# Kernel tuning notes

Measured on AMD Instinct MI355X. Metric: run time of the kernel, lower is better.

The kernel has to match this reference:

```python
import jax, jax.numpy as jnp
import numpy as np

EPS = 1e-5
NUM_GROUPS = 32

def _nin(x, w, b):
    # 1x1 conv: x (B,C,H,W), w (K,C), b (K,)
    return jnp.einsum('bchw,kc->bkhw', x, w) + b[None, :, None, None]

def _group_norm(x, gamma, beta, num_groups=NUM_GROUPS, eps=EPS):
    B, C, H, W = x.shape
    xg = x.reshape(B, num_groups, C // num_groups, H, W)
    mean = xg.mean(axis=(2, 3, 4), keepdims=True)
    var = xg.var(axis=(2, 3, 4), keepdims=True)
    xg = (xg - mean) * jax.lax.rsqrt(var + eps)
    x = xg.reshape(B, C, H, W)
    return x * gamma[None, :, None, None] + beta[None, :, None, None]

def setup_inputs() -> dict:
    key = jax.random.key(0)
    ks = jax.random.split(key, 10)
    B, C, H, W = 8, 512, 64, 64
    att = 512
    s = 0.02
    return {
        'x': jax.random.normal(ks[0], (B, C, H, W), dtype=jnp.float32),
        'gn_weight': jnp.ones((C,), jnp.float32),
        'gn_bias': jnp.zeros((C,), jnp.float32),
        'q_w': jax.random.normal(ks[1], (att, C), jnp.float32) * s,
        'q_b': jnp.zeros((att,), jnp.float32),
        'k_w': jax.random.normal(ks[2], (att, C), jnp.float32) * s,
        'k_b': jnp.zeros((att,), jnp.float32),
        'v_w': jax.random.normal(ks[3], (att, C), jnp.float32) * s,
        'v_b': jnp.zeros((att,), jnp.float32),
        'proj_w': jax.random.normal(ks[4], (C, att), jnp.float32) * s,
        'proj_b': jnp.zeros((C,), jnp.float32),
    }

def reference(x, gn_weight, gn_bias, q_w, q_b, k_w, k_b, v_w, v_b, proj_w, proj_b):
    B, C, H, W = x.shape
    h = _group_norm(x, gn_weight, gn_bias)
    q = _nin(h, q_w, q_b)  # (B, D, H, W)
    k = _nin(h, k_w, k_b)
    v = _nin(h, v_w, v_b)
    N = H * W
    qf = q.reshape(B, -1, N)
    kf = k.reshape(B, -1, N)
    vf = v.reshape(B, -1, N)
    scale = C ** (-0.5)  # note: scaled by input channel C, per source
    w = jnp.einsum('bdn,bdm->bnm', qf, kf) * scale  # (B, N, N)
    w = jax.nn.softmax(w, axis=-1)
    hf = jnp.einsum('bnm,bdm->bdn', w, vf)
    h = hf.reshape(B, -1, H, W)
    h = _nin(h, proj_w, proj_b)
    return x + h
```

## Files before the change

kernel.cpp:

```cpp
#include <hip/hip_runtime.h>
#include <hip/hip_bf16.h>
#include <cstdint>
#include <cstddef>

typedef __bf16 bf16_t;
typedef __bf16 bf16x8 __attribute__((ext_vector_type(8)));
typedef __bf16 bf16x4 __attribute__((ext_vector_type(4)));
typedef float f32x4 __attribute__((ext_vector_type(4)));

__device__ __forceinline__ void async16(const void* g, void* l) {
  __builtin_amdgcn_global_load_lds(
      (const __attribute__((address_space(1))) void*)g,
      (__attribute__((address_space(3))) void*)l,
      16, 0, 0);
}

__global__ __launch_bounds__(256) void f2b4(const float* __restrict__ w0,
                                            const float* __restrict__ w1,
                                            const float* __restrict__ w2,
                                            const float* __restrict__ w3,
                                            bf16_t* __restrict__ o0,
                                            bf16_t* __restrict__ o1,
                                            bf16_t* __restrict__ o2,
                                            bf16_t* __restrict__ o3) {
  const float* in = (blockIdx.y == 0) ? w0 : (blockIdx.y == 1) ? w1
                   : (blockIdx.y == 2) ? w2 : w3;
  bf16_t* out = (blockIdx.y == 0) ? o0 : (blockIdx.y == 1) ? o1
               : (blockIdx.y == 2) ? o2 : o3;
  const int i = blockIdx.x * 256 + threadIdx.x;
  float4 v = ((const float4*)in)[i];
  bf16x4 o = { (__bf16)v.x, (__bf16)v.y, (__bf16)v.z, (__bf16)v.w };
  ((bf16x4*)out)[i] = o;
}

__global__ __launch_bounds__(256) void groupnorm_t(const float* __restrict__ x,
                                                   const float* __restrict__ gamma,
                                                   const float* __restrict__ beta,
                                                   bf16_t* __restrict__ ht) {
  const int g = blockIdx.x;
  const int b = blockIdx.y;
  const int t = threadIdx.x;
  const float* xg = x + ((size_t)(b * 512 + g * 16)) * 4096;
  const float4* x4 = (const float4*)xg;

  float s = 0.f, ss = 0.f;
  #pragma unroll 8
  for (int i = t; i < 16384; i += 256) {
    float4 v = x4[i];
    s  += (v.x + v.y) + (v.z + v.w);
    ss += (v.x * v.x + v.y * v.y) + (v.z * v.z + v.w * v.w);
  }
  #pragma unroll
  for (int o = 32; o; o >>= 1) { s += __shfl_xor(s, o); ss += __shfl_xor(ss, o); }
  __shared__ float rs[4], rss[4];
  if ((t & 63) == 0) { rs[t >> 6] = s; rss[t >> 6] = ss; }
  __syncthreads();
  const float S  = (rs[0] + rs[1]) + (rs[2] + rs[3]);
  const float SS = (rss[0] + rss[1]) + (rss[2] + rss[3]);
  const float inv_n = 1.0f / 65536.0f;
  const float mean = S * inv_n;
  const float var  = SS * inv_n - mean * mean;
  const float rstd = rsqrtf(var + 1e-5f);

  float ga[16], be[16];
  #pragma unroll
  for (int cc = 0; cc < 16; cc++) {
    const float gm = gamma[g * 16 + cc] * rstd;
    ga[cc] = gm;
    be[cc] = beta[g * 16 + cc] - mean * gm;
  }

  bf16_t* hg = ht + (size_t)b * 4096 * 512 + g * 16;
  for (int n = t; n < 4096; n += 256) {
    bf16_t o[16];
    #pragma unroll
    for (int cc = 0; cc < 16; cc++)
      o[cc] = (bf16_t)(xg[(size_t)cc * 4096 + n] * ga[cc] + be[cc]);
    bf16x8* dst = (bf16x8*)(hg + (size_t)n * 512);
    dst[0] = *(bf16x8*)&o[0];
    dst[1] = *(bf16x8*)&o[8];
  }
}

template <int OUTF32, int BIAS_MODE, int RESID, int SWAP>
__global__ __launch_bounds__(256)
void gemm_bt(const bf16_t* __restrict__ A, const bf16_t* __restrict__ B,
             void* __restrict__ Cv, const float* __restrict__ bias,
             const float* __restrict__ resid,
             int TM, int TN, int Z, int K, float scale,
             long sA, long sB, long sC, long sR) {
  __shared__ alignas(16) bf16_t lA[4096];
  __shared__ alignas(16) bf16_t lB[4096];

  const int lid = blockIdx.x;
  const int xcd = lid & 7;
  const int j   = lid >> 3;
  const int sd  = SWAP ? TN : TM;
  const int I   = SWAP ? TM : TN;
  const int spx = (sd * Z) >> 3;
  const int strip = xcd * spx + j / I;
  const int inner = j % I;
  const int z    = strip / sd;
  const int sidx = strip % sd;
  const int bm = (SWAP ? inner : sidx) * 128;
  const int bn = (SWAP ? sidx : inner) * 128;
  const int N = TN * 128;

  const int t = threadIdx.x;
  const int lane = t & 63;
  const int w = t >> 6;
  const int wm = (w >> 1) * 64;
  const int wn = (w & 1) * 64;
  const bf16_t* Ab = A + (size_t)z * (size_t)sA;
  const bf16_t* Bb = B + (size_t)z * (size_t)sB;

  const int lrow = lane >> 2;
  const int lcol = (lane & 3) * 8;
  const int quad = lane >> 4;
  const int l15 = lane & 15;

  const bf16_t* gA0 = Ab + (size_t)(bm + w * 16 + lrow) * K + lcol;
  const bf16_t* gA1 = Ab + (size_t)(bm + (w + 4) * 16 + lrow) * K + lcol;
  const bf16_t* gB0 = Bb + (size_t)(bn + w * 16 + lrow) * K + lcol;
  const bf16_t* gB1 = Bb + (size_t)(bn + (w + 4) * 16 + lrow) * K + lcol;
  bf16_t* lA0 = &lA[w * 512];
  bf16_t* lA1 = &lA[(w + 4) * 512];
  bf16_t* lB0 = &lB[w * 512];
  bf16_t* lB1 = &lB[(w + 4) * 512];

  f32x4 acc[4][4] = {};

  for (int k0 = 0; k0 < K; k0 += 32) {
    __syncthreads();
    async16(gA0 + k0, lA0);
    async16(gA1 + k0, lA1);
    async16(gB0 + k0, lB0);
    async16(gB1 + k0, lB1);
    __syncthreads();

    bf16x8 af[4], bfr[4];
    #pragma unroll
    for (int i = 0; i < 4; i++) {
      af[i]  = *(const bf16x8*)&lA[(wm + i * 16 + l15) * 32 + quad * 8];
      bfr[i] = *(const bf16x8*)&lB[(wn + i * 16 + l15) * 32 + quad * 8];
    }
    #pragma unroll
    for (int i = 0; i < 4; i++)
      #pragma unroll
      for (int jj = 0; jj < 4; jj++)
        acc[i][jj] = __builtin_amdgcn_mfma_f32_16x16x32_bf16(af[i], bfr[jj],
                                                             acc[i][jj], 0, 0, 0);
  }

  float* Cf = (float*)Cv + (size_t)z * (size_t)sC;
  bf16_t* Cb = (bf16_t*)Cv + (size_t)z * (size_t)sC;
  const float* Rb = RESID ? (resid + (size_t)z * (size_t)sR) : nullptr;

  #pragma unroll
  for (int i = 0; i < 4; i++) {
    const int row0 = bm + wm + i * 16 + quad * 4;
    #pragma unroll
    for (int jj = 0; jj < 4; jj++) {
      const int col = bn + wn + jj * 16 + l15;
      #pragma unroll
      for (int r = 0; r < 4; r++) {
        float v = acc[i][jj][r] * scale;
        const int row = row0 + r;
        if (BIAS_MODE == 1) v += bias[row];
        else if (BIAS_MODE == 2) v += bias[col];
        const size_t idx = (size_t)row * N + col;
        if (RESID) v += Rb[idx];
        if (OUTF32) Cf[idx] = v;
        else Cb[idx] = (bf16_t)v;
      }
    }
  }
}

__global__ __launch_bounds__(512, 2)
void flash_attn(const bf16_t* __restrict__ Qm, const bf16_t* __restrict__ Km,
                const bf16_t* __restrict__ Vm, bf16_t* __restrict__ Om,
                float scale) {
  __shared__ alignas(16) bf16_t lT[2][4][128][32];
  __shared__ alignas(16) bf16_t lS[8][16][144];
  __shared__ float lL[8][16];

  const int bid = blockIdx.x;
  const int z = bid & 7;
  const int qb = bid >> 3;
  const int m0 = qb * 128;

  const int t = threadIdx.x;
  const int lane = t & 63;
  const int w = t >> 6;
  const int quad = lane >> 4;
  const int l15 = lane & 15;
  const int srow = lane >> 2;
  const int scol = (lane & 3) * 8;
  const int g2 = w & 6;
  const int dh = w & 1;

  const size_t sND = 4096ull * 512;
  const bf16_t* q = Qm + z * sND;
  const bf16_t* k = Km + z * sND;
  const bf16_t* v = Vm + z * sND;

  const bf16_t* kStage = k + (size_t)(w * 16 + srow) * 512 + scol;
  const bf16_t* vStage = v + (size_t)(w * 16 + srow) * 4096 + scol;

  bf16x8 qf[16];
  {
    const bf16_t* qrow = q + (size_t)(m0 + w * 16 + l15) * 512 + quad * 8;
    #pragma unroll
    for (int kk = 0; kk < 16; kk++)
      qf[kk] = *(const bf16x8*)(qrow + kk * 32);
  }

  f32x4 o_acc[32] = {};
  float l_run[4] = {0.f, 0.f, 0.f, 0.f};
  f32x4 s_acc[8];

  auto stageA = [&](int BUF, int kcc, int kd2) __attribute__((always_inline)) {
    #pragma unroll
    for (int c = 0; c < 4; c++)
      async16(kStage + (size_t)kcc * 512 + kd2 * 128 + c * 32,
              &lT[BUF][c][w * 16][0]);
  };
  auto stageC = [&](int BUF, int kcc, int db) __attribute__((always_inline)) {
    #pragma unroll
    for (int c = 0; c < 4; c++)
      async16(vStage + (size_t)db * 128 * 4096 + kcc + c * 32,
              &lT[BUF][c][w * 16][0]);
  };
  auto computeA = [&](int BUF, int kd2) __attribute__((always_inline)) {
    #pragma unroll
    for (int p = 0; p < 4; p++)
      #pragma unroll
      for (int n = 0; n < 8; n++) {
        bf16x8 kf = *(const bf16x8*)&lT[BUF][p][n * 16 + l15][quad * 8];
        s_acc[n] = __builtin_amdgcn_mfma_f32_16x16x32_bf16(
            qf[kd2 * 4 + p], kf, s_acc[n], 0, 0, 0);
      }
  };
  auto computeC = [&](int BUF, int db) __attribute__((always_inline)) {
    #pragma unroll
    for (int p = 0; p < 4; p++) {
      bf16x8 af0 = *(const bf16x8*)&lS[g2][l15][p * 32 + quad * 8];
      bf16x8 af1 = *(const bf16x8*)&lS[g2 + 1][l15][p * 32 + quad * 8];
      #pragma unroll
      for (int nd = 0; nd < 4; nd++) {
        bf16x8 vf = *(const bf16x8*)&lT[BUF][p][dh * 64 + nd * 16 + l15][quad * 8];
        o_acc[db * 8 + nd] = __builtin_amdgcn_mfma_f32_16x16x32_bf16(
            af0, vf, o_acc[db * 8 + nd], 0, 0, 0);
        o_acc[db * 8 + 4 + nd] = __builtin_amdgcn_mfma_f32_16x16x32_bf16(
            af1, vf, o_acc[db * 8 + 4 + nd], 0, 0, 0);
      }
    }
  };
  auto phaseB = [&]() __attribute__((always_inline)) {
    float lsum[4] = {0.f, 0.f, 0.f, 0.f};
    #pragma unroll
    for (int n = 0; n < 8; n++)
      #pragma unroll
      for (int r = 0; r < 4; r++) {
        float e = __expf(s_acc[n][r] * scale);
        lsum[r] += e;
        lS[w][quad * 4 + r][n * 16 + l15] = (bf16_t)e;
      }
    #pragma unroll
    for (int r = 0; r < 4; r++) {
      float s = lsum[r];
      s += __shfl_xor(s, 1); s += __shfl_xor(s, 2);
      s += __shfl_xor(s, 4); s += __shfl_xor(s, 8);
      l_run[r] += s;
    }
  };

  stageA(0, 0, 0);
  __syncthreads();

  for (int kc = 0; kc < 4096; kc += 128) {
    #pragma unroll
    for (int n = 0; n < 8; n++) s_acc[n] = (f32x4){0.f, 0.f, 0.f, 0.f};

    stageA(1, kc, 1);  computeA(0, 0);            __syncthreads();
    stageA(0, kc, 2);  computeA(1, 1);            __syncthreads();
    stageA(1, kc, 3);  computeA(0, 2);            __syncthreads();
    stageC(0, kc, 0);  computeA(1, 3);  phaseB(); __syncthreads();
    stageC(1, kc, 1);  computeC(0, 0);            __syncthreads();
    stageC(0, kc, 2);  computeC(1, 1);            __syncthreads();
    stageC(1, kc, 3);  computeC(0, 2);            __syncthreads();
    if (kc + 128 < 4096) stageA(0, kc + 128, 0);
    computeC(1, 3);                               __syncthreads();
  }

  if (l15 == 0) {
    #pragma unroll
    for (int r = 0; r < 4; r++) lL[w][quad * 4 + r] = l_run[r];
  }
  __syncthreads();
  float rl[2][4];
  #pragma unroll
  for (int s = 0; s < 2; s++)
    #pragma unroll
    for (int r = 0; r < 4; r++) rl[s][r] = 1.0f / lL[g2 + s][quad * 4 + r];

  bf16_t* o = Om + z * sND;
  #pragma unroll
  for (int db = 0; db < 4; db++)
    #pragma unroll
    for (int s = 0; s < 2; s++)
      #pragma unroll
      for (int nd = 0; nd < 4; nd++)
        #pragma unroll
        for (int r = 0; r < 4; r++) {
          const int row = m0 + (g2 + s) * 16 + quad * 4 + r;
          const int col = db * 128 + dh * 64 + nd * 16 + l15;
          o[(size_t)row * 512 + col] =
              (bf16_t)(o_acc[db * 8 + s * 4 + nd][r] * rl[s][r]);
        }
}

extern "C" void kernel_launch(void* const* d_in, const int* in_sizes, int n_in,
                              void* d_out, int out_size, void* d_ws, size_t ws_size,
                              hipStream_t stream) {
  const float* x   = (const float*)d_in[0];
  const float* gnw = (const float*)d_in[1];
  const float* gnb = (const float*)d_in[2];
  const float* qw  = (const float*)d_in[3];
  const float* qb  = (const float*)d_in[4];
  const float* kw  = (const float*)d_in[5];
  const float* kb  = (const float*)d_in[6];
  const float* vw  = (const float*)d_in[7];
  const float* vb  = (const float*)d_in[8];
  const float* pw  = (const float*)d_in[9];
  const float* pb  = (const float*)d_in[10];
  float* out = (float*)d_out;

  char* ws = (char*)d_ws;
  size_t off = 0;
  auto alloc = [&](size_t bytes) -> void* {
    void* p = ws + off;
    off += (bytes + 255) & ~(size_t)255;
    return p;
  };

  const long sND = 4096L * 512;

  bf16_t* wqb = (bf16_t*)alloc(512ull * 512 * 2);
  bf16_t* wkb = (bf16_t*)alloc(512ull * 512 * 2);
  bf16_t* wvb = (bf16_t*)alloc(512ull * 512 * 2);
  bf16_t* wpb = (bf16_t*)alloc(512ull * 512 * 2);
  bf16_t* ht  = (bf16_t*)alloc(8ull * 4096 * 512 * 2);
  bf16_t* qbf = (bf16_t*)alloc(8ull * 4096 * 512 * 2);
  bf16_t* kbf = (bf16_t*)alloc(8ull * 4096 * 512 * 2);
  bf16_t* vbf = (bf16_t*)alloc(8ull * 4096 * 512 * 2);
  bf16_t* hfb = ht;

  f2b4<<<dim3(256, 4), 256, 0, stream>>>(qw, kw, vw, pw, wqb, wkb, wvb, wpb);
  groupnorm_t<<<dim3(32, 8), 256, 0, stream>>>(x, gnw, gnb, ht);

  gemm_bt<0, 2, 0, 0><<<1024, 256, 0, stream>>>(
      ht, wqb, qbf, qb, nullptr, 32, 4, 8, 512, 1.0f, sND, 0, sND, 0);
  gemm_bt<0, 2, 0, 0><<<1024, 256, 0, stream>>>(
      ht, wkb, kbf, kb, nullptr, 32, 4, 8, 512, 1.0f, sND, 0, sND, 0);
  gemm_bt<0, 1, 0, 1><<<1024, 256, 0, stream>>>(
      wvb, ht, vbf, vb, nullptr, 4, 32, 8, 512, 1.0f, 0, sND, sND, 0);

  const float scale = 0.044194173824159216f;
  flash_attn<<<256, 512, 0, stream>>>(qbf, kbf, vbf, hfb, scale);

  gemm_bt<1, 1, 1, 1><<<1024, 256, 0, stream>>>(
      wpb, hfb, out, pb, x, 4, 32, 8, 512, 1.0f, 0, sND, 512L * 4096, 512L * 4096);
}
```

Baseline: 661.4 us.

## Split attention keys across two wave groups with smaller query tiles

The flash attention kernel now processes 64 query rows per block instead of 128 and splits each 128-key chunk between two groups of four waves, each holding its own half of the key/value tiles. Partial output accumulators and row sums are combined through shared memory at the end, and the grid doubles to 512 blocks. The score scratch is XOR-swizzled to avoid LDS bank conflicts. The intent is more blocks for better CU occupancy and load balance, at the cost of a shared-memory reduction epilogue, extra barriers, and Q being re-read by twice as many blocks.

After: 756.2 us. 1.14x slower.

```diff
diff --git a/kernel.cpp b/kernel.cpp
--- a/kernel.cpp
+++ b/kernel.cpp
@@ -181,20 +181,22 @@
 void flash_attn(const bf16_t* __restrict__ Qm, const bf16_t* __restrict__ Km,
                 const bf16_t* __restrict__ Vm, bf16_t* __restrict__ Om,
                 float scale) {
-  __shared__ alignas(16) bf16_t lT[2][4][128][32];
-  __shared__ alignas(16) bf16_t lS[8][16][144];
-  __shared__ float lL[8][16];
+  __shared__ alignas(16) bf16_t lT[2][2][8192];
+  __shared__ alignas(16) bf16_t lS[8][16][64];
 
   const int bid = blockIdx.x;
   const int z = bid & 7;
   const int qb = bid >> 3;
-  const int m0 = qb * 128;
+  const int m0 = qb * 64;
 
   const int t = threadIdx.x;
   const int lane = t & 63;
   const int w = t >> 6;
+  const int ws = w & 3;
+  const int kh = w >> 2;
   const int quad = lane >> 4;
   const int l15 = lane & 15;
+  const int l7 = l15 & 7;
   const int srow = lane >> 2;
   const int scol = (lane & 3) * 8;
   const int g2 = w & 6;
@@ -205,12 +207,12 @@
   const bf16_t* k = Km + z * sND;
   const bf16_t* v = Vm + z * sND;
 
-  const bf16_t* kStage = k + (size_t)(w * 16 + srow) * 512 + scol;
-  const bf16_t* vStage = v + (size_t)(w * 16 + srow) * 4096 + scol;
+  const bf16_t* kStage = k + (size_t)(ws * 16 + srow) * 512 + scol;
+  const bf16_t* vStage = v + (size_t)(ws * 32 + srow) * 4096 + scol;
 
   bf16x8 qf[16];
   {
-    const bf16_t* qrow = q + (size_t)(m0 + w * 16 + l15) * 512 + quad * 8;
+    const bf16_t* qrow = q + (size_t)(m0 + ws * 16 + l15) * 512 + quad * 8;
     #pragma unroll
     for (int kk = 0; kk < 16; kk++)
       qf[kk] = *(const bf16x8*)(qrow + kk * 32);
@@ -218,38 +220,45 @@
 
   f32x4 o_acc[32] = {};
   float l_run[4] = {0.f, 0.f, 0.f, 0.f};
-  f32x4 s_acc[8];
-
-  auto stageA = [&](int BUF, int kcc, int kd2) __attribute__((always_inline)) {
+  f32x4 s_acc[4];
+
+  bf16_t* myT0 = &lT[kh][0][0];
+  bf16_t* myT1 = &lT[kh][1][0];
+
+  auto stageA = [&](bf16_t* T, int kcc, int kd2) __attribute__((always_inline)) {
     #pragma unroll
     for (int c = 0; c < 4; c++)
       async16(kStage + (size_t)kcc * 512 + kd2 * 128 + c * 32,
-              &lT[BUF][c][w * 16][0]);
-  };
-  auto stageC = [&](int BUF, int kcc, int db) __attribute__((always_inline)) {
-    #pragma unroll
-    for (int c = 0; c < 4; c++)
+              T + c * 2048 + ws * 512);
+  };
+  auto stageC = [&](bf16_t* T, int kcc, int db) __attribute__((always_inline)) {
+    #pragma unroll
+    for (int c = 0; c < 2; c++) {
       async16(vStage + (size_t)db * 128 * 4096 + kcc + c * 32,
-              &lT[BUF][c][w * 16][0]);
-  };
-  auto computeA = [&](int BUF, int kd2) __attribute__((always_inline)) {
+              T + c * 4096 + ws * 1024);
+      async16(vStage + (size_t)(db * 128 + 16) * 4096 + kcc + c * 32,
+              T + c * 4096 + ws * 1024 + 512);
+    }
+  };
+  auto computeA = [&](const bf16_t* T, int kd2) __attribute__((always_inline)) {
     #pragma unroll
     for (int p = 0; p < 4; p++)
       #pragma unroll
-      for (int n = 0; n < 8; n++) {
-        bf16x8 kf = *(const bf16x8*)&lT[BUF][p][n * 16 + l15][quad * 8];
+      for (int n = 0; n < 4; n++) {
+        bf16x8 kf = *(const bf16x8*)&T[p * 2048 + (n * 16 + l15) * 32 + quad * 8];
         s_acc[n] = __builtin_amdgcn_mfma_f32_16x16x32_bf16(
             qf[kd2 * 4 + p], kf, s_acc[n], 0, 0, 0);
       }
   };
-  auto computeC = [&](int BUF, int db) __attribute__((always_inline)) {
-    #pragma unroll
-    for (int p = 0; p < 4; p++) {
-      bf16x8 af0 = *(const bf16x8*)&lS[g2][l15][p * 32 + quad * 8];
-      bf16x8 af1 = *(const bf16x8*)&lS[g2 + 1][l15][p * 32 + quad * 8];
+  auto computeC = [&](const bf16_t* T, int db) __attribute__((always_inline)) {
+    #pragma unroll
+    for (int p = 0; p < 2; p++) {
+      bf16x8 af0 = *(const bf16x8*)&lS[g2][l15][((p * 4 + quad) ^ l7) * 8];
+      bf16x8 af1 = *(const bf16x8*)&lS[g2 + 1][l15][((p * 4 + quad) ^ l7) * 8];
       #pragma unroll
       for (int nd = 0; nd < 4; nd++) {
-        bf16x8 vf = *(const bf16x8*)&lT[BUF][p][dh * 64 + nd * 16 + l15][quad * 8];
+        bf16x8 vf = *(const bf16x8*)
+            &T[p * 4096 + (dh * 64 + nd * 16 + l15) * 32 + quad * 8];
         o_acc[db * 8 + nd] = __builtin_amdgcn_mfma_f32_16x16x32_bf16(
             af0, vf, o_acc[db * 8 + nd], 0, 0, 0);
         o_acc[db * 8 + 4 + nd] = __builtin_amdgcn_mfma_f32_16x16x32_bf16(
@@ -260,12 +269,13 @@
   auto phaseB = [&]() __attribute__((always_inline)) {
     float lsum[4] = {0.f, 0.f, 0.f, 0.f};
     #pragma unroll
-    for (int n = 0; n < 8; n++)
+    for (int n = 0; n < 4; n++)
       #pragma unroll
       for (int r = 0; r < 4; r++) {
         float e = __expf(s_acc[n][r] * scale);
         lsum[r] += e;
-        lS[w][quad * 4 + r][n * 16 + l15] = (bf16_t)e;
+        const int row = quad * 4 + r;
+        lS[w][row][(((n * 2 + (l15 >> 3)) ^ (row & 7)) * 8) + l7] = (bf16_t)e;
       }
     #pragma unroll
     for (int r = 0; r < 4; r++) {
@@ -276,49 +286,77 @@
     }
   };
 
-  stageA(0, 0, 0);
-  __syncthreads();
-
-  for (int kc = 0; kc < 4096; kc += 128) {
-    #pragma unroll
-    for (int n = 0; n < 8; n++) s_acc[n] = (f32x4){0.f, 0.f, 0.f, 0.f};
-
-    stageA(1, kc, 1);  computeA(0, 0);            __syncthreads();
-    stageA(0, kc, 2);  computeA(1, 1);            __syncthreads();
-    stageA(1, kc, 3);  computeA(0, 2);            __syncthreads();
-    stageC(0, kc, 0);  computeA(1, 3);  phaseB(); __syncthreads();
-    stageC(1, kc, 1);  computeC(0, 0);            __syncthreads();
-    stageC(0, kc, 2);  computeC(1, 1);            __syncthreads();
-    stageC(1, kc, 3);  computeC(0, 2);            __syncthreads();
-    if (kc + 128 < 4096) stageA(0, kc + 128, 0);
-    computeC(1, 3);                               __syncthreads();
-  }
-
+  stageA(myT0, kh * 64, 0);
+  __syncthreads();
+
+  for (int i = 0; i < 32; i++) {
+    const int kc = i * 128 + kh * 64;
+    #pragma unroll
+    for (int n = 0; n < 4; n++) s_acc[n] = (f32x4){0.f, 0.f, 0.f, 0.f};
+
+    stageA(myT1, kc, 1);  computeA(myT0, 0);            __syncthreads();
+    stageA(myT0, kc, 2);  computeA(myT1, 1);            __syncthreads();
+    stageA(myT1, kc, 3);  computeA(myT0, 2);            __syncthreads();
+    stageC(myT0, kc, 0);  computeA(myT1, 3);  phaseB(); __syncthreads();
+    stageC(myT1, kc, 1);  computeC(myT0, 0);            __syncthreads();
+    stageC(myT0, kc, 2);  computeC(myT1, 1);            __syncthreads();
+    stageC(myT1, kc, 3);  computeC(myT0, 2);            __syncthreads();
+    if (i < 31) stageA(myT0, kc + 128, 0);
+    computeC(myT1, 3);                                  __syncthreads();
+  }
+
+  float* lLf = (float*)&lS[0][0][0];
   if (l15 == 0) {
     #pragma unroll
-    for (int r = 0; r < 4; r++) lL[w][quad * 4 + r] = l_run[r];
-  }
-  __syncthreads();
-  float rl[2][4];
-  #pragma unroll
-  for (int s = 0; s < 2; s++)
-    #pragma unroll
-    for (int r = 0; r < 4; r++) rl[s][r] = 1.0f / lL[g2 + s][quad * 4 + r];
-
-  bf16_t* o = Om + z * sND;
-  #pragma unroll
-  for (int db = 0; db < 4; db++)
+    for (int r = 0; r < 4; r++) lLf[w * 16 + quad * 4 + r] = l_run[r];
+  }
+  f32x4* fb = (f32x4*)&lT[0][0][0];
+  __syncthreads();
+  if (w == 4 || w == 5) {
+    #pragma unroll
+    for (int i = 0; i < 32; i++) fb[(w - 4) * 2048 + i * 64 + lane] = o_acc[i];
+  }
+  __syncthreads();
+  if (w == 0 || w == 1) {
+    #pragma unroll
+    for (int i = 0; i < 32; i++) o_acc[i] += fb[w * 2048 + i * 64 + lane];
+  }
+  __syncthreads();
+  if (w == 6 || w == 7) {
+    #pragma unroll
+    for (int i = 0; i < 32; i++) fb[(w - 6) * 2048 + i * 64 + lane] = o_acc[i];
+  }
+  __syncthreads();
+  if (w == 2 || w == 3) {
+    #pragma unroll
+    for (int i = 0; i < 32; i++) o_acc[i] += fb[(w - 2) * 2048 + i * 64 + lane];
+  }
+  __syncthreads();
+
+  if (w < 4) {
+    float rl[2][4];
     #pragma unroll
     for (int s = 0; s < 2; s++)
       #pragma unroll
-      for (int nd = 0; nd < 4; nd++)
+      for (int r = 0; r < 4; r++) {
+        const int idx = (g2 + s) * 16 + quad * 4 + r;
+        rl[s][r] = 1.0f / (lLf[idx] + lLf[idx + 64]);
+      }
+    bf16_t* o = Om + z * sND;
+    #pragma unroll
+    for (int db = 0; db < 4; db++)
+      #pragma unroll
+      for (int s = 0; s < 2; s++)
         #pragma unroll
-        for (int r = 0; r < 4; r++) {
-          const int row = m0 + (g2 + s) * 16 + quad * 4 + r;
-          const int col = db * 128 + dh * 64 + nd * 16 + l15;
-          o[(size_t)row * 512 + col] =
-              (bf16_t)(o_acc[db * 8 + s * 4 + nd][r] * rl[s][r]);
-        }
+        for (int nd = 0; nd < 4; nd++)
+          #pragma unroll
+          for (int r = 0; r < 4; r++) {
+            const int row = m0 + (g2 + s) * 16 + quad * 4 + r;
+            const int col = db * 128 + dh * 64 + nd * 16 + l15;
+            o[(size_t)row * 512 + col] =
+                (bf16_t)(o_acc[db * 8 + s * 4 + nd][r] * rl[s][r]);
+          }
+  }
 }
 
 extern "C" void kernel_launch(void* const* d_in, const int* in_sizes, int n_in,
@@ -368,7 +406,7 @@
       wvb, ht, vbf, vb, nullptr, 4, 32, 8, 512, 1.0f, 0, sND, sND, 0);
 
   const float scale = 0.044194173824159216f;
-  flash_attn<<<256, 512, 0, stream>>>(qbf, kbf, vbf, hfb, scale);
+  flash_attn<<<512, 512, 0, stream>>>(qbf, kbf, vbf, hfb, scale);
 
   gemm_bt<1, 1, 1, 1><<<1024, 256, 0, stream>>>(
       wpb, hfb, out, pb, x, 4, 32, 8, 512, 1.0f, 0, sND, 512L * 4096, 512L * 4096);
```
